# Optimization experiments

Hardware: AMD Instinct MI355X
Metric: run time of the kernel (lower is better)

The kernel has to match this reference:

```python
import jax, jax.numpy as jnp
import numpy as np

Q, N, C, H, W = 200, 25, 640, 5, 5
TEMPERATURE = 0.1
EPS = 1e-8  # torch F.cosine_similarity eps


def setup_inputs() -> dict:
    key = jax.random.key(0)
    k1, k2 = jax.random.split(key)
    feature_q = jax.random.normal(k1, (Q, N, C, H, W), dtype=jnp.float32)
    feature_s = jax.random.normal(k2, (Q, N, C, H, W), dtype=jnp.float32)
    return {"feature_q": feature_q, "feature_s": feature_s}


def reference(feature_q, feature_s):
    # Correlation volume: contract over channels c -> [Q, N, Hs, Ws, Hq, Wq]
    corr = jnp.einsum('qncij,qnckl->qnijkl', feature_s, feature_q)

    # Co-attention: mean-pool over the opposite spatial dims, softmax over last axis
    s_att = jax.nn.softmax(corr.mean(axis=(4, 5)), axis=-1)  # [Q, N, Hs, Ws]
    q_att = jax.nn.softmax(corr.mean(axis=(2, 3)), axis=-1)  # [Q, N, Hq, Wq]

    # Support aggregation (mode='support'):
    # torch broadcast [1,Q,N,1,H,W]*[1,Q,N,C,H,W] then mean(dim=1)
    # == mean over q of s_att[q,n,h,w] * feature_s[q,n,c,h,w] -> [1,N,C,H,W]
    attended_s = (s_att[:, :, None, :, :] * feature_s).mean(axis=0, keepdims=True)

    # Query aggregation (mode='query'):
    # torch broadcast [1,Q',N,1,H,W]*[Q,1,N,C,H,W] then mean(dim=1=Q')
    # == feature_q[q,n,c,h,w] * mean_{q'} q_att[q',n,h,w] -> [Q,N,C,H,W]
    # (fused form: avoids materializing the [Q,Q,N,C,H,W] intermediate)
    attended_q = feature_q * q_att.mean(axis=0)[None, :, None, :, :]

    # Cosine similarity along last dim (W), torch semantics with eps clamp
    dot = jnp.sum(attended_s * attended_q, axis=-1)               # [Q,N,C,H]
    norm_s = jnp.maximum(jnp.sqrt(jnp.sum(attended_s * attended_s, axis=-1)), EPS)
    norm_q = jnp.maximum(jnp.sqrt(jnp.sum(attended_q * attended_q, axis=-1)), EPS)
    similarity_score = dot / (norm_s * norm_q) / TEMPERATURE      # [Q,N,C,H]
    return similarity_score
```

## Files before the change

kernel.cpp:

```cpp
#include <hip/hip_runtime.h>

constexpr int Qn = 200;
constexpr int Nn = 25;
constexpr int Cn = 640;
constexpr int Hn = 5;
constexpr int Wn = 5;
constexpr int HWn = Hn * Wn;
constexpr int CHW = Cn * HWn;
constexpr float TEMP_INV = 10.0f;
constexpr float EPSC = 1e-8f;

__global__ __launch_bounds__(256) void attn_kernel(
    const float* __restrict__ fq, const float* __restrict__ fs,
    float* __restrict__ s_att, float* __restrict__ qbar)
{
    const int qn = blockIdx.x;
    const int n  = qn % Nn;
    const float* fq_t = fq + (size_t)qn * CHW;
    const float* fs_t = fs + (size_t)qn * CHW;

    float ms[HWn], mq[HWn];
#pragma unroll
    for (int p = 0; p < HWn; ++p) { ms[p] = 0.f; mq[p] = 0.f; }

    const int tid = threadIdx.x;
    for (int c = tid; c < Cn; c += 256) {
        const float* fqr = fq_t + c * HWn;
        const float* fsr = fs_t + c * HWn;
        float vq[HWn], vs[HWn];
        float sq = 0.f, ss = 0.f;
#pragma unroll
        for (int p = 0; p < HWn; ++p) { vq[p] = fqr[p]; sq += vq[p]; }
#pragma unroll
        for (int p = 0; p < HWn; ++p) { vs[p] = fsr[p]; ss += vs[p]; }
#pragma unroll
        for (int p = 0; p < HWn; ++p) {
            ms[p] += vs[p] * sq;
            mq[p] += vq[p] * ss;
        }
    }

    __shared__ float red[4 * 2 * HWn];
    __shared__ float fm[2 * HWn];
    const int lane = tid & 63;
    const int wave = tid >> 6;
#pragma unroll
    for (int p = 0; p < HWn; ++p) {
        float v = ms[p];
        v += __shfl_down(v, 32); v += __shfl_down(v, 16); v += __shfl_down(v, 8);
        v += __shfl_down(v, 4);  v += __shfl_down(v, 2);  v += __shfl_down(v, 1);
        if (lane == 0) red[wave * (2 * HWn) + p] = v;
        float u = mq[p];
        u += __shfl_down(u, 32); u += __shfl_down(u, 16); u += __shfl_down(u, 8);
        u += __shfl_down(u, 4);  u += __shfl_down(u, 2);  u += __shfl_down(u, 1);
        if (lane == 0) red[wave * (2 * HWn) + HWn + p] = u;
    }
    __syncthreads();
    if (tid < 2 * HWn) {
        fm[tid] = red[tid] + red[2 * HWn + tid] + red[4 * HWn + tid] + red[6 * HWn + tid];
    }
    __syncthreads();

    if (tid < 10) {
        const int r = tid;
        const float* row = (r < 5) ? &fm[r * 5] : &fm[HWn + (r - 5) * 5];
        float v[5];
        float mx = -1e30f;
#pragma unroll
        for (int j = 0; j < 5; ++j) {
            v[j] = row[j] * (1.0f / HWn);
            mx = fmaxf(mx, v[j]);
        }
        float s = 0.f;
#pragma unroll
        for (int j = 0; j < 5; ++j) { v[j] = __expf(v[j] - mx); s += v[j]; }
        const float inv = 1.0f / s;
        if (r < 5) {
#pragma unroll
            for (int j = 0; j < 5; ++j)
                s_att[(size_t)qn * HWn + r * 5 + j] = v[j] * inv;
        } else {
#pragma unroll
            for (int j = 0; j < 5; ++j)
                atomicAdd(&qbar[n * HWn + (r - 5) * 5 + j],
                          v[j] * inv * (1.0f / Qn));
        }
    }
}

__global__ __launch_bounds__(256) void agg_kernel(
    const float* __restrict__ fs, const float* __restrict__ s_att,
    float* __restrict__ att_s)
{
    const int n = blockIdx.y;
    const int f = blockIdx.x * 256 + threadIdx.x;
    if (f >= CHW) return;
    const int hw = f % HWn;
    float acc = 0.f;
    for (int q = 0; q < Qn; ++q) {
        const int qn = q * Nn + n;
        const float w = s_att[(size_t)qn * HWn + hw];
        acc += w * fs[(size_t)qn * CHW + f];
    }
    att_s[(size_t)n * CHW + f] = acc * (1.0f / Qn);
}

__global__ __launch_bounds__(256) void cos_kernel(
    const float* __restrict__ fq, const float* __restrict__ att_s,
    const float* __restrict__ qbar, float* __restrict__ out)
{
    const size_t idx = (size_t)blockIdx.x * 256 + threadIdx.x;
    if (idx >= (size_t)Qn * Nn * Cn * Hn) return;
    const int h = (int)(idx % Hn);
    const size_t t = idx / Hn;
    const int c = (int)(t % Cn);
    const size_t qn = t / Cn;
    const int n = (int)(qn % Nn);

    const float* fqr = fq + (qn * Cn + c) * HWn + h * Wn;
    const float* asr = att_s + ((size_t)n * Cn + c) * HWn + h * Wn;
    const float* qb  = qbar + n * HWn + h * Wn;

    float dot = 0.f, ns2 = 0.f, nq2 = 0.f;
#pragma unroll
    for (int w = 0; w < Wn; ++w) {
        const float aq = fqr[w] * qb[w];
        const float as = asr[w];
        dot += as * aq;
        ns2 += as * as;
        nq2 += aq * aq;
    }
    const float ns = fmaxf(sqrtf(ns2), EPSC);
    const float nq = fmaxf(sqrtf(nq2), EPSC);
    out[idx] = dot / (ns * nq) * TEMP_INV;
}

extern "C" void kernel_launch(void* const* d_in, const int* in_sizes, int n_in,
                              void* d_out, int out_size, void* d_ws, size_t ws_size,
                              hipStream_t stream)
{
    const float* fq = (const float*)d_in[0];
    const float* fs = (const float*)d_in[1];
    float* out = (float*)d_out;

    float* s_att = (float*)d_ws;
    float* qbar  = s_att + (size_t)Qn * Nn * HWn;
    float* att_s = qbar + 1024;

    hipMemsetAsync(qbar, 0, Nn * HWn * sizeof(float), stream);

    attn_kernel<<<Qn * Nn, 256, 0, stream>>>(fq, fs, s_att, qbar);

    dim3 g2((CHW + 255) / 256, Nn);
    agg_kernel<<<g2, 256, 0, stream>>>(fs, s_att, att_s);

    const size_t total = (size_t)Qn * Nn * Cn * Hn;
    cos_kernel<<<(unsigned)((total + 255) / 256), 256, 0, stream>>>(fq, att_s, qbar, out);
}
```

Before: 779.9 us.

## Stage attn tiles via global_load_lds and split agg over Q chunks with atomics

The attention kernel now brings each wave's 64-channel tile of both feature tensors into LDS using direct global-to-LDS loads, which gives fully coalesced 16-byte transfers before the per-channel reduction. The aggregation kernel now processes float4 elements, keeps the attention weights in LDS, and splits the Q dimension into 5 chunks that are combined with atomicAdd. Splitting Q this way raises parallelism, at the cost of zeroing the att_s buffer with a memset and paying for atomics. The LDS-staged attn path waits on vmcnt synchronously, so a single wave gets no overlap between loading and computing.

```diff
diff --git a/kernel.cpp b/kernel.cpp
--- a/kernel.cpp
+++ b/kernel.cpp
@@ -10,54 +10,84 @@
 constexpr float TEMP_INV = 10.0f;
 constexpr float EPSC = 1e-8f;
 
+typedef const float __attribute__((address_space(1)))* gbl_f;
+typedef float __attribute__((address_space(3)))* lds_f;
+
+__device__ __forceinline__ float wave_sum(float v) {
+    v += __shfl_down(v, 32); v += __shfl_down(v, 16); v += __shfl_down(v, 8);
+    v += __shfl_down(v, 4);  v += __shfl_down(v, 2);  v += __shfl_down(v, 1);
+    return v;
+}
+
 __global__ __launch_bounds__(256) void attn_kernel(
     const float* __restrict__ fq, const float* __restrict__ fs,
     float* __restrict__ s_att, float* __restrict__ qbar)
 {
-    const int qn = blockIdx.x;
-    const int n  = qn % Nn;
+    __shared__ float lds[4 * 3200];
+
+    const int qn   = blockIdx.x;
+    const int n    = qn % Nn;
+    const int tid  = threadIdx.x;
+    const int lane = tid & 63;
+    const int wave = tid >> 6;
+
     const float* fq_t = fq + (size_t)qn * CHW;
     const float* fs_t = fs + (size_t)qn * CHW;
+    float* ldsq = &lds[wave * 3200];
+    float* ldss = ldsq + 1600;
 
     float ms[HWn], mq[HWn];
 #pragma unroll
     for (int p = 0; p < HWn; ++p) { ms[p] = 0.f; mq[p] = 0.f; }
 
-    const int tid = threadIdx.x;
-    for (int c = tid; c < Cn; c += 256) {
-        const float* fqr = fq_t + c * HWn;
-        const float* fsr = fs_t + c * HWn;
+    for (int tile = wave; tile < 10; tile += 4) {
+        const float* gq = fq_t + tile * 1600;
+        const float* gs = fs_t + tile * 1600;
+
+        asm volatile("s_waitcnt lgkmcnt(0)" ::: "memory");
+
+#pragma unroll
+        for (int i = 0; i < 6; ++i) {
+            __builtin_amdgcn_global_load_lds((gbl_f)(gq + (i * 64 + lane) * 4),
+                                             (lds_f)(ldsq + i * 256), 16, 0, 0);
+            __builtin_amdgcn_global_load_lds((gbl_f)(gs + (i * 64 + lane) * 4),
+                                             (lds_f)(ldss + i * 256), 16, 0, 0);
+        }
+        __builtin_amdgcn_global_load_lds((gbl_f)(gq + 1536 + lane),
+                                         (lds_f)(ldsq + 1536), 4, 0, 0);
+        __builtin_amdgcn_global_load_lds((gbl_f)(gs + 1536 + lane),
+                                         (lds_f)(ldss + 1536), 4, 0, 0);
+        asm volatile("s_waitcnt vmcnt(0)" ::: "memory");
+
+        const float* rq = ldsq + lane * HWn;
+        const float* rs = ldss + lane * HWn;
         float vq[HWn], vs[HWn];
-        float sq = 0.f, ss = 0.f;
-#pragma unroll
-        for (int p = 0; p < HWn; ++p) { vq[p] = fqr[p]; sq += vq[p]; }
-#pragma unroll
-        for (int p = 0; p < HWn; ++p) { vs[p] = fsr[p]; ss += vs[p]; }
+        float sq = 0.f, ssv = 0.f;
+#pragma unroll
+        for (int p = 0; p < HWn; ++p) { vq[p] = rq[p]; sq += vq[p]; }
+#pragma unroll
+        for (int p = 0; p < HWn; ++p) { vs[p] = rs[p]; ssv += vs[p]; }
 #pragma unroll
         for (int p = 0; p < HWn; ++p) {
             ms[p] += vs[p] * sq;
-            mq[p] += vq[p] * ss;
-        }
-    }
-
-    __shared__ float red[4 * 2 * HWn];
-    __shared__ float fm[2 * HWn];
-    const int lane = tid & 63;
-    const int wave = tid >> 6;
+            mq[p] += vq[p] * ssv;
+        }
+    }
+
+    __syncthreads();
+
+    float* red = lds;
+    float* fm  = lds + 200;
 #pragma unroll
     for (int p = 0; p < HWn; ++p) {
-        float v = ms[p];
-        v += __shfl_down(v, 32); v += __shfl_down(v, 16); v += __shfl_down(v, 8);
-        v += __shfl_down(v, 4);  v += __shfl_down(v, 2);  v += __shfl_down(v, 1);
-        if (lane == 0) red[wave * (2 * HWn) + p] = v;
-        float u = mq[p];
-        u += __shfl_down(u, 32); u += __shfl_down(u, 16); u += __shfl_down(u, 8);
-        u += __shfl_down(u, 4);  u += __shfl_down(u, 2);  u += __shfl_down(u, 1);
-        if (lane == 0) red[wave * (2 * HWn) + HWn + p] = u;
-    }
-    __syncthreads();
-    if (tid < 2 * HWn) {
-        fm[tid] = red[tid] + red[2 * HWn + tid] + red[4 * HWn + tid] + red[6 * HWn + tid];
+        float v = wave_sum(ms[p]);
+        if (lane == 0) red[wave * 50 + p] = v;
+        float u = wave_sum(mq[p]);
+        if (lane == 0) red[wave * 50 + HWn + p] = u;
+    }
+    __syncthreads();
+    if (tid < 50) {
+        fm[tid] = red[tid] + red[50 + tid] + red[100 + tid] + red[150 + tid];
     }
     __syncthreads();
 
@@ -92,17 +122,40 @@
     const float* __restrict__ fs, const float* __restrict__ s_att,
     float* __restrict__ att_s)
 {
-    const int n = blockIdx.y;
-    const int f = blockIdx.x * 256 + threadIdx.x;
-    if (f >= CHW) return;
-    const int hw = f % HWn;
-    float acc = 0.f;
-    for (int q = 0; q < Qn; ++q) {
-        const int qn = q * Nn + n;
-        const float w = s_att[(size_t)qn * HWn + hw];
-        acc += w * fs[(size_t)qn * CHW + f];
-    }
-    att_s[(size_t)n * CHW + f] = acc * (1.0f / Qn);
+    constexpr int QCH = 40;
+    __shared__ float w_lds[QCH * HWn];
+    const int n  = blockIdx.y;
+    const int q0 = blockIdx.z * QCH;
+
+    for (int i = threadIdx.x; i < QCH * HWn; i += 256) {
+        const int q = q0 + i / HWn;
+        const int hw = i % HWn;
+        w_lds[i] = s_att[(size_t)(q * Nn + n) * HWn + hw];
+    }
+    __syncthreads();
+
+    const int f4 = blockIdx.x * 256 + threadIdx.x;
+    if (f4 >= CHW / 4) return;
+    const int f = f4 * 4;
+    const int hw0 = f % HWn, hw1 = (f + 1) % HWn,
+              hw2 = (f + 2) % HWn, hw3 = (f + 3) % HWn;
+
+    float4 acc = make_float4(0.f, 0.f, 0.f, 0.f);
+#pragma unroll 4
+    for (int qi = 0; qi < QCH; ++qi) {
+        const int q = q0 + qi;
+        const float4 v = *(const float4*)(fs + (size_t)(q * Nn + n) * CHW + f);
+        const float* w = &w_lds[qi * HWn];
+        acc.x += w[hw0] * v.x;
+        acc.y += w[hw1] * v.y;
+        acc.z += w[hw2] * v.z;
+        acc.w += w[hw3] * v.w;
+    }
+    float* dst = att_s + (size_t)n * CHW + f;
+    atomicAdd(dst + 0, acc.x * (1.0f / Qn));
+    atomicAdd(dst + 1, acc.y * (1.0f / Qn));
+    atomicAdd(dst + 2, acc.z * (1.0f / Qn));
+    atomicAdd(dst + 3, acc.w * (1.0f / Qn));
 }
 
 __global__ __launch_bounds__(256) void cos_kernel(
@@ -147,11 +200,11 @@
     float* qbar  = s_att + (size_t)Qn * Nn * HWn;
     float* att_s = qbar + 1024;
 
-    hipMemsetAsync(qbar, 0, Nn * HWn * sizeof(float), stream);
+    hipMemsetAsync(qbar, 0, (1024 + (size_t)Nn * CHW) * sizeof(float), stream);
 
     attn_kernel<<<Qn * Nn, 256, 0, stream>>>(fq, fs, s_att, qbar);
 
-    dim3 g2((CHW + 255) / 256, Nn);
+    dim3 g2((CHW / 4 + 255) / 256, Nn, 5);
     agg_kernel<<<g2, 256, 0, stream>>>(fs, s_att, att_s);
 
     const size_t total = (size_t)Qn * Nn * Cn * Hn;
```

Measured after the change: 775.5 us. About the same (-0.6%).
